# Kernel optimization log

Hardware: AMD Instinct MI355X
Metric: run time of the kernel (lower is better)

## Reference

```python
import jax, jax.numpy as jnp
import numpy as np

B, C, N, K = 4, 192, 8192, 16
C_OUT = 192


def _gather_nodes(xs, idx):
    # xs: [B, C, N], idx: [B, N, K] -> [B, C, N, K]
    return jax.vmap(lambda xb, ib: xb[:, ib])(xs, idx)


def setup_inputs() -> dict:
    key = jax.random.key(0)
    k1, k2, k3 = jax.random.split(key, 3)
    x = jax.random.normal(k1, (B, C, N, 1), dtype=jnp.float32)
    x_0 = jnp.zeros((B, C, N, 1), dtype=jnp.float32)  # unused by forward, kept for interface
    edge_index = jax.random.randint(k2, (2, B, N, K), 0, N, dtype=jnp.int32)
    # 1x1 Conv2d(2C -> C_OUT) weight flattened to [C_OUT, 2C]
    W = jax.random.normal(k3, (C_OUT, 2 * C), dtype=jnp.float32) / np.sqrt(2 * C)
    b = jnp.zeros((C_OUT,), dtype=jnp.float32)
    return {"x": x, "x_0": x_0, "edge_index": edge_index, "W": W, "b": b}


def reference(x, x_0, edge_index, W, b):
    xs = x[..., 0]                       # [B, C, N]
    x_i = _gather_nodes(xs, edge_index[1])   # centers  [B, C, N, K]
    x_j = _gather_nodes(xs, edge_index[0])   # neighbors [B, C, N, K]
    rel = jnp.max(x_j - x_i, axis=-1)        # max-relative [B, C, N]
    y = jnp.concatenate([xs, rel], axis=1)   # [B, 2C, N]
    out = jnp.einsum('oc,bcn->bon', W, y) + b[None, :, None]  # 1x1 conv
    out = jax.nn.relu(out)
    return out[..., None]                # [B, C_OUT, N, 1]
```

## Files before the change

kernel.cpp:

```cpp
#include <hip/hip_runtime.h>
#include <hip/hip_fp16.h>

#define B_    4
#define C_    192
#define N_    8192
#define K_    16
#define O_    192
#define TWOC_ 384

typedef __attribute__((ext_vector_type(8))) _Float16 half8;
typedef __attribute__((ext_vector_type(4))) _Float16 half4v;
typedef __attribute__((ext_vector_type(4))) float floatx4;

#define NINF ((_Float16)(-65504.0f))

__global__ __launch_bounds__(256) void k_convert_w(const float* __restrict__ W,
                                                   unsigned short* __restrict__ Wb) {
    int i = blockIdx.x * 256 + threadIdx.x;
    if (i < O_ * TWOC_) {
        union { _Float16 h; unsigned short s; } v;
        v.h = (_Float16)W[i];
        Wb[i] = v.s;
    }
}

__global__ __launch_bounds__(256) void k_transpose(const float* __restrict__ x,
                                                   unsigned short* __restrict__ xt) {
    __shared__ float tile[32][33];
    int bid  = blockIdx.x;
    int xcd  = bid & 7;
    int b    = xcd >> 1;
    int half = xcd & 1;
    int slot = bid >> 3;
    int ct   = slot >> 7;
    int nt   = half * 128 + (slot & 127);
    int c0 = ct * 32, n0 = nt * 32;
    int tid = threadIdx.x;

    int cc  = tid >> 3;
    int nn4 = (tid & 7) * 4;
    const float* xp = x + ((size_t)b * C_ + c0 + cc) * N_ + n0 + nn4;
    float4 v = *(const float4*)xp;
    tile[nn4 + 0][cc] = v.x;
    tile[nn4 + 1][cc] = v.y;
    tile[nn4 + 2][cc] = v.z;
    tile[nn4 + 3][cc] = v.w;
    __syncthreads();

#pragma unroll
    for (int i = 0; i < 2; i++) {
        int id  = i * 256 + tid;
        int row = id >> 4;
        int ch2 = id & 15;
        union { _Float16 h[2]; unsigned int u; } p;
        p.h[0] = (_Float16)tile[row][ch2 * 2];
        p.h[1] = (_Float16)tile[row][ch2 * 2 + 1];
        *(unsigned int*)(xt + ((size_t)b * N_ + n0 + row) * C_ + c0 + ch2 * 2) = p.u;
    }
}

__global__ __launch_bounds__(256, 4) void k_fused(const unsigned short* __restrict__ xt,
                                                  const int* __restrict__ eidx,
                                                  const unsigned short* __restrict__ Wb,
                                                  const float* __restrict__ bias,
                                                  float* __restrict__ out) {
    __shared__ __align__(16) unsigned short rtile[32][192];
    __shared__ int sidx[32][33];

    int bid  = blockIdx.x;
    int xcd  = bid & 7;
    int b    = xcd >> 1;
    int slot = bid >> 3;
    int n0   = ((xcd & 1) * 128 + slot) * 32;

    int tid  = threadIdx.x;
    int wave = tid >> 6;
    int lane = tid & 63;
    int m16  = lane & 15;
    int quad = lane >> 4;

    const int* e0 = eidx + ((size_t)b * N_ + n0) * K_;
    const int* e1 = e0 + (size_t)B_ * N_ * K_;
#pragma unroll
    for (int i = 0; i < 2; i++) {
        int id = i * 256 + tid;
        int node = id >> 4, k = id & 15;
        sidx[node][k]      = e0[id];
        sidx[node][16 + k] = e1[id];
    }

    floatx4 acc[3][2];
#pragma unroll
    for (int i = 0; i < 3; i++)
#pragma unroll
        for (int j = 0; j < 2; j++) acc[i][j] = (floatx4){0.f, 0.f, 0.f, 0.f};

    const unsigned short* wbase = Wb + (size_t)(wave * 48 + m16) * TWOC_ + quad * 8;
    const unsigned short* ybase = xt + ((size_t)b * N_ + n0 + m16) * C_ + quad * 8;

#pragma unroll 2
    for (int kt = 0; kt < 6; kt++) {
        half8 wf[3], yf[2];
#pragma unroll
        for (int i = 0; i < 3; i++)
            wf[i] = *(const half8*)(wbase + (size_t)(i * 16) * TWOC_ + kt * 32);
#pragma unroll
        for (int j = 0; j < 2; j++)
            yf[j] = *(const half8*)(ybase + (size_t)(j * 16) * C_ + kt * 32);
#pragma unroll
        for (int i = 0; i < 3; i++)
#pragma unroll
            for (int j = 0; j < 2; j++)
                acc[i][j] = __builtin_amdgcn_mfma_f32_16x16x32_f16(wf[i], yf[j], acc[i][j], 0, 0, 0);
    }

    __syncthreads();

    {
        const unsigned short* xbase = xt + (size_t)b * N_ * C_;
        int g = quad, l4 = m16;
#pragma unroll
        for (int bb = 0; bb < 2; bb++) {
            int node = wave * 8 + bb * 4 + g;
            half8  m0 = {NINF, NINF, NINF, NINF, NINF, NINF, NINF, NINF};
            half4v m1 = {NINF, NINF, NINF, NINF};
#pragma unroll
            for (int k = 0; k < K_; k++) {
                int jn  = sidx[node][k];
                int in_ = sidx[node][16 + k];
                const unsigned short* pj = xbase + (size_t)jn * C_;
                const unsigned short* pi = xbase + (size_t)in_ * C_;
                half8  a0 = *(const half8*)(pj + l4 * 8);
                half8  b0 = *(const half8*)(pi + l4 * 8);
                half4v a1 = *(const half4v*)(pj + 128 + l4 * 4);
                half4v b1 = *(const half4v*)(pi + 128 + l4 * 4);
                m0 = __builtin_elementwise_max(m0, a0 - b0);
                m1 = __builtin_elementwise_max(m1, a1 - b1);
            }
            char* rb = (char*)rtile + node * 384;
            unsigned int sw = (unsigned)(node & 7) << 4;
            *(half8*)(rb + ((unsigned)(l4 * 16) ^ sw))        = m0;
            *(half4v*)(rb + ((unsigned)(256 + l4 * 8) ^ sw))  = m1;
        }
    }
    __syncthreads();

#pragma unroll 2
    for (int kt = 0; kt < 6; kt++) {
        half8 wf[3], yf[2];
#pragma unroll
        for (int i = 0; i < 3; i++)
            wf[i] = *(const half8*)(wbase + (size_t)(i * 16) * TWOC_ + (C_ + kt * 32));
#pragma unroll
        for (int j = 0; j < 2; j++) {
            int r = j * 16 + m16;
            unsigned int off = (unsigned)(kt * 64 + quad * 16) ^ ((unsigned)(r & 7) << 4);
            yf[j] = *(const half8*)((char*)rtile + (size_t)r * 384 + off);
        }
#pragma unroll
        for (int i = 0; i < 3; i++)
#pragma unroll
            for (int j = 0; j < 2; j++)
                acc[i][j] = __builtin_amdgcn_mfma_f32_16x16x32_f16(wf[i], yf[j], acc[i][j], 0, 0, 0);
    }

#pragma unroll
    for (int i = 0; i < 3; i++) {
#pragma unroll
        for (int r = 0; r < 4; r++) {
            int o = wave * 48 + i * 16 + quad * 4 + r;
            float bv = bias[o];
#pragma unroll
            for (int j = 0; j < 2; j++) {
                int n = n0 + j * 16 + m16;
                out[((size_t)b * O_ + o) * N_ + n] = fmaxf(acc[i][j][r] + bv, 0.f);
            }
        }
    }
}

extern "C" void kernel_launch(void* const* d_in, const int* in_sizes, int n_in,
                              void* d_out, int out_size, void* d_ws, size_t ws_size,
                              hipStream_t stream) {
    const float* x    = (const float*)d_in[0];
    const int*   eidx = (const int*)d_in[2];
    const float* W    = (const float*)d_in[3];
    const float* bias = (const float*)d_in[4];
    float*       out  = (float*)d_out;

    unsigned short* Wb = (unsigned short*)d_ws;
    unsigned short* xt = (unsigned short*)((char*)d_ws + 147456);

    k_convert_w<<<dim3((O_ * TWOC_ + 255) / 256), dim3(256), 0, stream>>>(W, Wb);
    k_transpose<<<dim3(6144), dim3(256), 0, stream>>>(x, xt);
    k_fused<<<dim3(1024), dim3(256), 0, stream>>>(xt, eidx, Wb, bias, out);
}
```

Baseline: 139.3 us.

## Split fused gather+conv into separate gather and conv kernels

Unfuses the max-relative gather from the 1x1 conv. A new gather kernel spreads each node's 16 neighbors across lane groups, reduces with xor shuffles, and writes the rel features to a workspace buffer. A separate conv kernel stages 64-node x 384-channel tiles in LDS and runs the full MFMA GEMM over larger tiles. The aim is more memory-level parallelism in the gather and better GEMM reuse, at the cost of an extra global write and read of the rel tensor plus one more launch.

```diff
diff --git a/kernel.cpp b/kernel.cpp
--- a/kernel.cpp
+++ b/kernel.cpp
@@ -7,12 +7,26 @@
 #define K_    16
 #define O_    192
 #define TWOC_ 384
+#define BN_   (B_ * N_)
 
 typedef __attribute__((ext_vector_type(8))) _Float16 half8;
 typedef __attribute__((ext_vector_type(4))) _Float16 half4v;
 typedef __attribute__((ext_vector_type(4))) float floatx4;
 
-#define NINF ((_Float16)(-65504.0f))
+static __device__ __forceinline__ half8 shflx8(half8 v, int m) {
+    union { half8 h; int i[4]; } u;
+    u.h = v;
+#pragma unroll
+    for (int q = 0; q < 4; q++) u.i[q] = __shfl_xor(u.i[q], m, 64);
+    return u.h;
+}
+static __device__ __forceinline__ half4v shflx4(half4v v, int m) {
+    union { half4v h; int i[2]; } u;
+    u.h = v;
+#pragma unroll
+    for (int q = 0; q < 2; q++) u.i[q] = __shfl_xor(u.i[q], m, 64);
+    return u.h;
+}
 
 __global__ __launch_bounds__(256) void k_convert_w(const float* __restrict__ W,
                                                    unsigned short* __restrict__ Wb) {
@@ -59,19 +73,77 @@
     }
 }
 
-__global__ __launch_bounds__(256, 4) void k_fused(const unsigned short* __restrict__ xt,
-                                                  const int* __restrict__ eidx,
-                                                  const unsigned short* __restrict__ Wb,
-                                                  const float* __restrict__ bias,
-                                                  float* __restrict__ out) {
-    __shared__ __align__(16) unsigned short rtile[32][192];
-    __shared__ int sidx[32][33];
+__global__ __launch_bounds__(256) void k_gather(const unsigned short* __restrict__ xt,
+                                                const int* __restrict__ eidx,
+                                                unsigned short* __restrict__ rt) {
+    int tid  = threadIdx.x;
+    int lane = tid & 63;
+    int w    = tid >> 6;
+    int part = lane & 15;
+    int kg   = lane >> 4;
+
+    int bid  = blockIdx.x;
+    int xcd  = bid & 7;
+    int b    = xcd >> 1;
+    int half = xcd & 1;
+    int slot = bid >> 3;
+    int widx = slot * 4 + w;
+    int nbase = half * 4096 + widx * 4;
+
+    const unsigned short* xb = xt + (size_t)b * N_ * C_;
+    const int* e0 = eidx + ((size_t)b * N_ + nbase) * K_;
+    const int* e1 = e0 + (size_t)BN_ * K_;
+
+#pragma unroll
+    for (int nn = 0; nn < 4; nn++) {
+        int4 j4 = *(const int4*)(e0 + nn * K_ + kg * 4);
+        int4 i4 = *(const int4*)(e1 + nn * K_ + kg * 4);
+        half8  m0;
+        half4v m1;
+#pragma unroll
+        for (int it = 0; it < 4; it++) {
+            int jn  = (it == 0) ? j4.x : (it == 1) ? j4.y : (it == 2) ? j4.z : j4.w;
+            int in_ = (it == 0) ? i4.x : (it == 1) ? i4.y : (it == 2) ? i4.z : i4.w;
+            const unsigned short* pj = xb + (size_t)jn * C_;
+            const unsigned short* pi = xb + (size_t)in_ * C_;
+            half8  a0 = *(const half8*)(pj + part * 8);
+            half4v a1 = *(const half4v*)(pj + 128 + part * 4);
+            half8  b0 = *(const half8*)(pi + part * 8);
+            half4v b1 = *(const half4v*)(pi + 128 + part * 4);
+            half8  d0 = a0 - b0;
+            half4v d1 = a1 - b1;
+            if (it == 0) { m0 = d0; m1 = d1; }
+            else {
+                m0 = __builtin_elementwise_max(m0, d0);
+                m1 = __builtin_elementwise_max(m1, d1);
+            }
+        }
+        m0 = __builtin_elementwise_max(m0, shflx8(m0, 16));
+        m1 = __builtin_elementwise_max(m1, shflx4(m1, 16));
+        m0 = __builtin_elementwise_max(m0, shflx8(m0, 32));
+        m1 = __builtin_elementwise_max(m1, shflx4(m1, 32));
+
+        if (kg == 0) {
+            unsigned short* ro = rt + ((size_t)b * N_ + nbase + nn) * C_;
+            *(half8*)(ro + part * 8)        = m0;
+            *(half4v*)(ro + 128 + part * 4) = m1;
+        }
+    }
+}
+
+__global__ __launch_bounds__(256) void k_conv(const unsigned short* __restrict__ xt,
+                                              const unsigned short* __restrict__ rt,
+                                              const unsigned short* __restrict__ Wb,
+                                              const float* __restrict__ bias,
+                                              float* __restrict__ out) {
+    __shared__ __align__(16) unsigned short ytile[64 * TWOC_];
+    char* yb = (char*)ytile;
 
     int bid  = blockIdx.x;
     int xcd  = bid & 7;
     int b    = xcd >> 1;
     int slot = bid >> 3;
-    int n0   = ((xcd & 1) * 128 + slot) * 32;
+    int n0   = ((xcd & 1) * 64 + slot) * 64;
 
     int tid  = threadIdx.x;
     int wave = tid >> 6;
@@ -79,88 +151,43 @@
     int m16  = lane & 15;
     int quad = lane >> 4;
 
-    const int* e0 = eidx + ((size_t)b * N_ + n0) * K_;
-    const int* e1 = e0 + (size_t)B_ * N_ * K_;
-#pragma unroll
-    for (int i = 0; i < 2; i++) {
+    const unsigned short* xsrc = xt + ((size_t)b * N_ + n0) * C_;
+    const unsigned short* rsrc = rt + ((size_t)b * N_ + n0) * C_;
+#pragma unroll
+    for (int i = 0; i < 6; i++) {
         int id = i * 256 + tid;
-        int node = id >> 4, k = id & 15;
-        sidx[node][k]      = e0[id];
-        sidx[node][16 + k] = e1[id];
-    }
-
-    floatx4 acc[3][2];
+        int row = id / 24, chunk = id % 24;
+        int sw = (row & 7) << 4;
+        half8 vx = *(const half8*)(xsrc + (size_t)row * C_ + chunk * 8);
+        half8 vr = *(const half8*)(rsrc + (size_t)row * C_ + chunk * 8);
+        *(half8*)(yb + row * 768 + ((chunk * 16) ^ sw))       = vx;
+        *(half8*)(yb + row * 768 + 384 + ((chunk * 16) ^ sw)) = vr;
+    }
+    __syncthreads();
+
+    const unsigned short* wbase = Wb + (size_t)(wave * 48 + m16) * TWOC_ + quad * 8;
+
+    floatx4 acc[3][4];
 #pragma unroll
     for (int i = 0; i < 3; i++)
 #pragma unroll
-        for (int j = 0; j < 2; j++) acc[i][j] = (floatx4){0.f, 0.f, 0.f, 0.f};
-
-    const unsigned short* wbase = Wb + (size_t)(wave * 48 + m16) * TWOC_ + quad * 8;
-    const unsigned short* ybase = xt + ((size_t)b * N_ + n0 + m16) * C_ + quad * 8;
+        for (int j = 0; j < 4; j++) acc[i][j] = (floatx4){0.f, 0.f, 0.f, 0.f};
 
 #pragma unroll 2
-    for (int kt = 0; kt < 6; kt++) {
-        half8 wf[3], yf[2];
+    for (int kt = 0; kt < 12; kt++) {
+        half8 wf[3], yf[4];
 #pragma unroll
         for (int i = 0; i < 3; i++)
             wf[i] = *(const half8*)(wbase + (size_t)(i * 16) * TWOC_ + kt * 32);
 #pragma unroll
-        for (int j = 0; j < 2; j++)
-            yf[j] = *(const half8*)(ybase + (size_t)(j * 16) * C_ + kt * 32);
+        for (int j = 0; j < 4; j++) {
+            int row = j * 16 + m16;
+            yf[j] = *(const half8*)(yb + row * 768 + ((kt * 64 + quad * 16) ^ ((row & 7) << 4)));
+        }
 #pragma unroll
         for (int i = 0; i < 3; i++)
 #pragma unroll
-            for (int j = 0; j < 2; j++)
-                acc[i][j] = __builtin_amdgcn_mfma_f32_16x16x32_f16(wf[i], yf[j], acc[i][j], 0, 0, 0);
-    }
-
-    __syncthreads();
-
-    {
-        const unsigned short* xbase = xt + (size_t)b * N_ * C_;
-        int g = quad, l4 = m16;
-#pragma unroll
-        for (int bb = 0; bb < 2; bb++) {
-            int node = wave * 8 + bb * 4 + g;
-            half8  m0 = {NINF, NINF, NINF, NINF, NINF, NINF, NINF, NINF};
-            half4v m1 = {NINF, NINF, NINF, NINF};
-#pragma unroll
-            for (int k = 0; k < K_; k++) {
-                int jn  = sidx[node][k];
-                int in_ = sidx[node][16 + k];
-                const unsigned short* pj = xbase + (size_t)jn * C_;
-                const unsigned short* pi = xbase + (size_t)in_ * C_;
-                half8  a0 = *(const half8*)(pj + l4 * 8);
-                half8  b0 = *(const half8*)(pi + l4 * 8);
-                half4v a1 = *(const half4v*)(pj + 128 + l4 * 4);
-                half4v b1 = *(const half4v*)(pi + 128 + l4 * 4);
-                m0 = __builtin_elementwise_max(m0, a0 - b0);
-                m1 = __builtin_elementwise_max(m1, a1 - b1);
-            }
-            char* rb = (char*)rtile + node * 384;
-            unsigned int sw = (unsigned)(node & 7) << 4;
-            *(half8*)(rb + ((unsigned)(l4 * 16) ^ sw))        = m0;
-            *(half4v*)(rb + ((unsigned)(256 + l4 * 8) ^ sw))  = m1;
-        }
-    }
-    __syncthreads();
-
-#pragma unroll 2
-    for (int kt = 0; kt < 6; kt++) {
-        half8 wf[3], yf[2];
-#pragma unroll
-        for (int i = 0; i < 3; i++)
-            wf[i] = *(const half8*)(wbase + (size_t)(i * 16) * TWOC_ + (C_ + kt * 32));
-#pragma unroll
-        for (int j = 0; j < 2; j++) {
-            int r = j * 16 + m16;
-            unsigned int off = (unsigned)(kt * 64 + quad * 16) ^ ((unsigned)(r & 7) << 4);
-            yf[j] = *(const half8*)((char*)rtile + (size_t)r * 384 + off);
-        }
-#pragma unroll
-        for (int i = 0; i < 3; i++)
-#pragma unroll
-            for (int j = 0; j < 2; j++)
+            for (int j = 0; j < 4; j++)
                 acc[i][j] = __builtin_amdgcn_mfma_f32_16x16x32_f16(wf[i], yf[j], acc[i][j], 0, 0, 0);
     }
 
@@ -171,7 +198,7 @@
             int o = wave * 48 + i * 16 + quad * 4 + r;
             float bv = bias[o];
 #pragma unroll
-            for (int j = 0; j < 2; j++) {
+            for (int j = 0; j < 4; j++) {
                 int n = n0 + j * 16 + m16;
                 out[((size_t)b * O_ + o) * N_ + n] = fmaxf(acc[i][j][r] + bv, 0.f);
             }
@@ -190,8 +217,10 @@
 
     unsigned short* Wb = (unsigned short*)d_ws;
     unsigned short* xt = (unsigned short*)((char*)d_ws + 147456);
+    unsigned short* rt = (unsigned short*)((char*)d_ws + 12730368);
 
     k_convert_w<<<dim3((O_ * TWOC_ + 255) / 256), dim3(256), 0, stream>>>(W, Wb);
     k_transpose<<<dim3(6144), dim3(256), 0, stream>>>(x, xt);
-    k_fused<<<dim3(1024), dim3(256), 0, stream>>>(xt, eidx, Wb, bias, out);
-}
+    k_gather<<<dim3(2048), dim3(256), 0, stream>>>(xt, eidx, rt);
+    k_conv<<<dim3(512), dim3(256), 0, stream>>>(xt, rt, Wb, bias, out);
+}
```

Result: faster. 135.9 us (-2.4%).
